# Kernel optimization log

Hardware: AMD Instinct MI355X
Metric: run time of the kernel (lower is better)

## Reference

```python
import jax, jax.numpy as jnp
import numpy as np

A = -0.75  # torch bicubic coefficient
K = 5
K2 = K * K
IN_CH = 32 * 2 + 169 + 16 * 2 + 1  # 266
TIMESTEP = 0.5


def _cubic_w(t):
    # t in [0,1); weights for taps at offsets -1,0,1,2 (torch cubic convolution, A=-0.75)
    w1 = ((A + 2.0) * t - (A + 3.0)) * t * t + 1.0
    s = 1.0 - t
    w2 = ((A + 2.0) * s - (A + 3.0)) * s * s + 1.0
    u = t + 1.0
    w0 = ((A * u - 5.0 * A) * u + 8.0 * A) * u - 4.0 * A
    v = 2.0 - t
    w3 = ((A * v - 5.0 * A) * v + 8.0 * A) * v - 4.0 * A
    return (w0, w1, w2, w3)


def _conv3(x, w, b):
    y = jax.lax.conv_general_dilated(x, w, (1, 1), 'SAME',
                                     dimension_numbers=('NCHW', 'OIHW', 'NCHW'))
    return y + b[None, :, None, None]


def _lrelu(x):
    return jnp.where(x >= 0, x, 0.1 * x)


def _kernel_pred(x, w1, b1, w2, b2, w3, b3, ow, ob, ww, wb):
    f = _lrelu(_conv3(x, w1, b1))
    f = _lrelu(_conv3(f, w2, b2))
    f = _lrelu(_conv3(f, w3, b3))
    offsets = _conv3(f, ow, ob)                      # (B, 2*K2, H, W)
    weights = jax.nn.softmax(_conv3(f, ww, wb), axis=1)  # (B, K2, H, W)
    return offsets, weights


def _adacof_sample(image, offsets, weights):
    # bicubic grid_sample(padding_mode='border', align_corners=True) + weighted combine
    b, c, h, w = image.shape
    k2 = weights.shape[1]
    gx = jnp.arange(w, dtype=image.dtype)
    gy = jnp.arange(h, dtype=image.dtype)
    dx = offsets[:, 0::2]                # (b,k2,h,w)
    dy = offsets[:, 1::2]
    # with align_corners=True, normalize->unnormalize is identity
    sx = gx[None, None, None, :] + dx
    sy = gy[None, None, :, None] + dy
    x0 = jnp.floor(sx); tx = sx - x0
    y0 = jnp.floor(sy); ty = sy - y0
    wx = _cubic_w(tx)
    wy = _cubic_w(ty)
    xi = [jnp.clip(x0 + (i - 1.0), 0, w - 1).astype(jnp.int32) for i in range(4)]
    yi = [jnp.clip(y0 + (i - 1.0), 0, h - 1).astype(jnp.int32) for i in range(4)]
    imgf = image.reshape(b, c, h * w)
    gather = jax.vmap(lambda im, idx: im[:, idx])   # (c,hw),(n,)->(c,n)
    acc = jnp.zeros((b, c, k2, h, w), image.dtype)
    for i in range(4):
        for j in range(4):
            idx = (yi[i] * w + xi[j]).reshape(b, -1)
            g = gather(imgf, idx).reshape(b, c, k2, h, w)
            acc = acc + g * (wy[i] * wx[j])[:, None]
    return jnp.einsum('bckhw,bkhw->bchw', acc, weights)


def setup_inputs() -> dict:
    key = jax.random.key(0)
    ks = iter(jax.random.split(key, 64))
    d = {}
    d['frame1'] = jax.random.normal(next(ks), (2, 3, 256, 256), jnp.float32)
    d['frame2'] = jax.random.normal(next(ks), (2, 3, 256, 256), jnp.float32)
    d['feat1'] = jax.random.normal(next(ks), (2, 32, 256, 256), jnp.float32)
    d['feat2'] = jax.random.normal(next(ks), (2, 32, 256, 256), jnp.float32)
    d['corr'] = jax.random.normal(next(ks), (2, 169, 256, 256), jnp.float32)

    def conv_w(o, i):
        return jax.random.normal(next(ks), (o, i, 3, 3), jnp.float32) * 0.05

    # full-res encoder
    d['fr_w1'] = conv_w(16, 3); d['fr_b1'] = jnp.zeros((16,), jnp.float32)
    d['fr_w2'] = conv_w(16, 16); d['fr_b2'] = jnp.zeros((16,), jnp.float32)
    # default grid offsets for offset_head bias (dx,dy interleaved)
    off_bias = []
    for i in range(K):
        for j in range(K):
            off_bias.extend([j - K // 2, i - K // 2])
    off_bias = jnp.asarray(off_bias, jnp.float32)
    for p in ('kp1', 'kp2'):
        d[p + '_w1'] = conv_w(256, IN_CH); d[p + '_b1'] = jnp.zeros((256,), jnp.float32)
        d[p + '_w2'] = conv_w(256, 256); d[p + '_b2'] = jnp.zeros((256,), jnp.float32)
        d[p + '_w3'] = conv_w(128, 256); d[p + '_b3'] = jnp.zeros((128,), jnp.float32)
        d[p + '_ow'] = jax.random.normal(next(ks), (2 * K2, 128, 3, 3), jnp.float32) * 0.01
        d[p + '_ob'] = off_bias
        d[p + '_ww'] = jax.random.normal(next(ks), (K2, 128, 3, 3), jnp.float32) * 0.01
        d[p + '_wb'] = jnp.full((K2,), 1.0 / K2, jnp.float32)
    d['bl_w1'] = conv_w(64, IN_CH); d['bl_b1'] = jnp.zeros((64,), jnp.float32)
    d['bl_w2'] = conv_w(1, 64); d['bl_b2'] = jnp.zeros((1,), jnp.float32)
    return d


def reference(frame1, frame2, feat1, feat2, corr,
              fr_w1, fr_b1, fr_w2, fr_b2,
              kp1_w1, kp1_b1, kp1_w2, kp1_b2, kp1_w3, kp1_b3, kp1_ow, kp1_ob, kp1_ww, kp1_wb,
              kp2_w1, kp2_b1, kp2_w2, kp2_b2, kp2_w3, kp2_b3, kp2_ow, kp2_ob, kp2_ww, kp2_wb,
              bl_w1, bl_b1, bl_w2, bl_b2):
    b, _, h, w = frame1.shape
    fr1 = _lrelu(_conv3(_lrelu(_conv3(frame1, fr_w1, fr_b1)), fr_w2, fr_b2))
    fr2 = _lrelu(_conv3(_lrelu(_conv3(frame2, fr_w1, fr_b1)), fr_w2, fr_b2))
    t_map = jnp.full((b, 1, h, w), TIMESTEP, frame1.dtype)
    combined = jnp.concatenate([feat1, feat2, corr, fr1, fr2, t_map], axis=1)
    offsets1, weights1 = _kernel_pred(combined, kp1_w1, kp1_b1, kp1_w2, kp1_b2,
                                      kp1_w3, kp1_b3, kp1_ow, kp1_ob, kp1_ww, kp1_wb)
    offsets2, weights2 = _kernel_pred(combined, kp2_w1, kp2_b1, kp2_w2, kp2_b2,
                                      kp2_w3, kp2_b3, kp2_ow, kp2_ob, kp2_ww, kp2_wb)
    sample1 = _adacof_sample(frame1, offsets1, weights1)
    sample2 = _adacof_sample(frame2, offsets2, weights2)
    blend = jax.nn.sigmoid(_conv3(_lrelu(_conv3(combined, bl_w1, bl_b1)), bl_w2, bl_b2))
    output = blend * sample1 + (1.0 - blend) * sample2
    return (output, blend, offsets1, offsets2, weights1, weights2)
```

## Files before the change

kernel.cpp:

```cpp
#include <hip/hip_runtime.h>
#include <cstdint>
#include <cstddef>

#define H 256
#define W 256
#define HW (H*W)
#define BATCH 2
#define CIN_TILE 4

typedef __bf16 bf16x8 __attribute__((ext_vector_type(8)));
typedef float f32x4 __attribute__((ext_vector_type(4)));
typedef __attribute__((address_space(1))) uint32_t gu32_t;
typedef __attribute__((address_space(3))) uint32_t lu32_t;

__device__ __forceinline__ void async16(const void* g, void* l) {
  __builtin_amdgcn_global_load_lds((const gu32_t*)g, (lu32_t*)l, 16, 0, 0);
}

__device__ __forceinline__ ushort f2bf(float f) {
  uint u = __float_as_uint(f);
  return (ushort)((u + 0x7FFFu + ((u >> 16) & 1u)) >> 16);
}
__device__ __forceinline__ float lrelu_f(float v) { return v >= 0.f ? v : 0.1f * v; }

#define SWN (2304 * 8)
#define SBN (4 * 640 * 8)
#define DYN_LDS_BYTES (2 * (SWN + SBN) * 2)

#define ISSUE_TAP(tt, bb)                                                     \
  do {                                                                        \
    asm volatile("ds_read_b128 %0, %1 offset:%c2"                             \
                 : "=v"(Afr[bb][0]) : "v"(aA0), "i"((tt) * 4096));            \
    asm volatile("ds_read_b128 %0, %1 offset:%c2"                             \
                 : "=v"(Afr[bb][1]) : "v"(aA1), "i"((tt) * 4096));            \
    asm volatile("ds_read_b128 %0, %1 offset:%c2"                             \
                 : "=v"(Afr[bb][2]) : "v"(aA2), "i"((tt) * 4096));            \
    asm volatile("ds_read_b128 %0, %1 offset:%c2"                             \
                 : "=v"(Afr[bb][3]) : "v"(aA3), "i"((tt) * 4096));            \
    asm volatile("ds_read_b128 %0, %1 offset:%c2"                             \
                 : "=v"(Bfr[bb][0]) : "v"(aB0),                               \
                   "i"(((((tt) / 3) * 34) + ((tt) % 3)) * 16));               \
    asm volatile("ds_read_b128 %0, %1 offset:%c2"                             \
                 : "=v"(Bfr[bb][1]) : "v"(aB1),                               \
                   "i"(((((tt) / 3) * 34) + ((tt) % 3)) * 16));               \
    asm volatile("ds_read_b128 %0, %1 offset:%c2"                             \
                 : "=v"(Bfr[bb][2]) : "v"(aB2),                               \
                   "i"(((((tt) / 3) * 34) + ((tt) % 3)) * 16));               \
    asm volatile("ds_read_b128 %0, %1 offset:%c2"                             \
                 : "=v"(Bfr[bb][3]) : "v"(aB3),                               \
                   "i"(((((tt) / 3) * 34) + ((tt) % 3)) * 16));               \
  } while (0)

template<int EPI>
__global__ __launch_bounds__(512) void convmm_k(
    const ushort* __restrict__ act, const ushort* __restrict__ wgt,
    const float* __restrict__ bias, ushort* __restrict__ dstb,
    float* __restrict__ dsto, float* __restrict__ dstw,
    const ushort* __restrict__ zpage, int Cin, int CoutS,
    int astride, int wstride, int bstride, int dstride)
{
  extern __shared__ __align__(16) ushort s_dyn[];

  const int z = blockIdx.z;
  act += (size_t)z * astride;
  wgt += (size_t)z * wstride;
  bias += (size_t)z * bstride;
  if constexpr (EPI == 0) dstb += (size_t)z * dstride;
  else { dsto += (size_t)z * (BATCH * 50 * HW); dstw += (size_t)z * (BATCH * 25 * HW); }

  const int tid = threadIdx.x;
  const int sp = blockIdx.x;
  const int bx = (sp & 7) * 32, by = (sp >> 3) * 16;
  const int co0 = blockIdx.y * 64;
  const int wv = tid >> 6, lane = tid & 63;
  const int c = lane & 15, kq = lane >> 4;
  const int oy = wv * 2;

  int wsrc[5];
#pragma unroll
  for (int it = 0; it < 5; ++it) {
    int i = tid + it * 512;
    if (i < 2304) {
      int co = i & 63, tk = i >> 6, tap = tk >> 2, kg = tk & 3;
      wsrc[it] = ((co0 + co) * 9 + tap) * Cin + kg * 8;
    } else wsrc[it] = 0;
  }
  int bsrc[5];
#pragma unroll
  for (int it = 0; it < 5; ++it) {
    int i = tid + it * 512;
    int kg = i / 640, px = i - kg * 640;
    int row = px / 34, xx = px - row * 34;
    int gy = by + row - 1, gx = bx + xx - 1;
    bool ok = (px < 612) && ((unsigned)gy < (unsigned)H) && ((unsigned)gx < (unsigned)W);
    bsrc[it] = ok ? ((gy * W + gx) * Cin + kg * 8) : -1;
  }

  auto stage = [&](int buf, int c0) {
    ushort* swc = s_dyn + (buf ? (SWN + SBN) : 0);
    ushort* sbc = swc + SWN;
#pragma unroll
    for (int it = 0; it < 5; ++it)
      if (it < 4 || tid < 2304 - 4 * 512)
        async16(wgt + wsrc[it] + c0, &swc[(size_t)(tid + it * 512) * 8]);
#pragma unroll
    for (int it = 0; it < 5; ++it) {
      const ushort* g = (bsrc[it] < 0) ? zpage : (act + bsrc[it] + c0);
      async16(g, &sbc[(size_t)(tid + it * 512) * 8]);
    }
  };

  f32x4 acc[4][4];
#pragma unroll
  for (int a = 0; a < 4; ++a)
#pragma unroll
    for (int b2 = 0; b2 < 4; ++b2) acc[a][b2] = (f32x4){0.f, 0.f, 0.f, 0.f};

  stage(0, 0);
  __syncthreads();

  const uint sdyn_base = (uint)(uintptr_t)(lu32_t*)s_dyn;

  const int nch = Cin >> 5;
  int cur = 0;
  for (int ch = 0; ch < nch; ++ch) {
    if (ch + 1 < nch) stage(cur ^ 1, (ch + 1) << 5);
    __builtin_amdgcn_sched_barrier(0);

    const uint swoff = sdyn_base + (cur ? (uint)((SWN + SBN) * 2) : 0u);
    const uint sboff = swoff + (uint)(SWN * 2);
    const uint aA0 = swoff + (uint)((kq * 64 + 0 * 16 + c) * 16);
    const uint aA1 = swoff + (uint)((kq * 64 + 1 * 16 + c) * 16);
    const uint aA2 = swoff + (uint)((kq * 64 + 2 * 16 + c) * 16);
    const uint aA3 = swoff + (uint)((kq * 64 + 3 * 16 + c) * 16);
    const uint aB0 = sboff + (uint)((kq * 640 + (oy + 0) * 34 + 0 * 16 + c) * 16);
    const uint aB1 = sboff + (uint)((kq * 640 + (oy + 0) * 34 + 1 * 16 + c) * 16);
    const uint aB2 = sboff + (uint)((kq * 640 + (oy + 1) * 34 + 0 * 16 + c) * 16);
    const uint aB3 = sboff + (uint)((kq * 640 + (oy + 1) * 34 + 1 * 16 + c) * 16);

    bf16x8 Afr[2][4], Bfr[2][4];
    ISSUE_TAP(0, 0);

#pragma unroll
    for (int t = 0; t < 9; ++t) {
      if (t < 8) {
        switch (t + 1) {
          case 1: ISSUE_TAP(1, 1); break;
          case 2: ISSUE_TAP(2, 0); break;
          case 3: ISSUE_TAP(3, 1); break;
          case 4: ISSUE_TAP(4, 0); break;
          case 5: ISSUE_TAP(5, 1); break;
          case 6: ISSUE_TAP(6, 0); break;
          case 7: ISSUE_TAP(7, 1); break;
          case 8: ISSUE_TAP(8, 0); break;
        }
        asm volatile("s_waitcnt lgkmcnt(8)" ::: "memory");
      } else {
        asm volatile("s_waitcnt lgkmcnt(0)" ::: "memory");
      }
      __builtin_amdgcn_sched_barrier(0);
      __builtin_amdgcn_s_setprio(1);
#pragma unroll
      for (int cf = 0; cf < 4; ++cf) {
#pragma unroll
        for (int pf = 0; pf < 4; ++pf)
          acc[cf][pf] = __builtin_amdgcn_mfma_f32_16x16x32_bf16(
              Afr[t & 1][cf], Bfr[t & 1][pf], acc[cf][pf], 0, 0, 0);
      }
      __builtin_amdgcn_s_setprio(0);
      __builtin_amdgcn_sched_barrier(0);
    }

    __syncthreads();
    cur ^= 1;
  }

  const int r4 = kq * 4;
#pragma unroll
  for (int cf = 0; cf < 4; ++cf) {
    int cob = co0 + cf * 16 + r4;
#pragma unroll
    for (int pf = 0; pf < 4; ++pf) {
      int gx2 = bx + (pf & 1) * 16 + c;
      int gy2 = by + oy + (pf >> 1);
      int gpix = gy2 * W + gx2;
      f32x4 v = acc[cf][pf];
      const float4 bv = *(const float4*)&bias[cob];
      if constexpr (EPI == 0) {
        ushort4 ov;
        float f0 = lrelu_f(v[0] + bv.x);
        float f1 = lrelu_f(v[1] + bv.y);
        float f2 = lrelu_f(v[2] + bv.z);
        float f3 = lrelu_f(v[3] + bv.w);
        ov.x = f2bf(f0); ov.y = f2bf(f1); ov.z = f2bf(f2); ov.w = f2bf(f3);
        *(ushort4*)&dstb[(size_t)gpix * CoutS + cob] = ov;
      } else {
        const float* bvp = &bv.x;
#pragma unroll
        for (int r = 0; r < 4; ++r) {
          int coa = cob + r;
          if (coa < 75) {
            float f = v[r] + bvp[r];
            if (coa < 50) dsto[(size_t)coa * HW + gpix] = f;
            else          dstw[(size_t)(coa - 50) * HW + gpix] = f;
          }
        }
      }
    }
  }
}

template<int CIN>
__global__ __launch_bounds__(256) void conv_fr_k(
    const float* __restrict__ sA, const float* __restrict__ sB, int mode,
    const float* __restrict__ wgt, const float* __restrict__ bias,
    float* __restrict__ dst)
{
  const int z = blockIdx.y;
  const float* src = (mode == 0)
      ? (((z >> 1) ? sB : sA) + (size_t)(z & 1) * 3 * HW)
      : (sA + (size_t)z * 16 * HW);
  float* out = dst + (size_t)z * 16 * HW;

  const int sp = blockIdx.x;
  const int bx = (sp & 7) * 32, by = (sp >> 3) * 32;
  const int tid = threadIdx.x;
  const int tx = tid & 15, ty = tid >> 4;

  __shared__ float s_in[CIN_TILE][34][36];
  float acc[16][2][2];
#pragma unroll
  for (int co = 0; co < 16; ++co) {
    acc[co][0][0] = 0.f; acc[co][0][1] = 0.f;
    acc[co][1][0] = 0.f; acc[co][1][1] = 0.f;
  }

  for (int c0 = 0; c0 < CIN; c0 += CIN_TILE) {
    __syncthreads();
    const int nst = CIN_TILE * 34 * 34;
    for (int i = tid; i < nst; i += 256) {
      int ci = i / (34 * 34);
      int r = i - ci * (34 * 34);
      int yy = r / 34;
      int xx = r - yy * 34;
      int gy = by + yy - 1, gx = bx + xx - 1;
      int cc = c0 + ci;
      float v = 0.f;
      if (cc < CIN && (unsigned)gy < (unsigned)H && (unsigned)gx < (unsigned)W)
        v = src[(size_t)cc * HW + gy * W + gx];
      s_in[ci][yy][xx] = v;
    }
    __syncthreads();

    const int cmax = (CIN - c0 < CIN_TILE) ? (CIN - c0) : CIN_TILE;
    for (int ci = 0; ci < cmax; ++ci) {
      float win[4][4];
#pragma unroll
      for (int iy = 0; iy < 4; ++iy)
#pragma unroll
        for (int ix = 0; ix < 4; ++ix)
          win[iy][ix] = s_in[ci][2 * ty + iy][2 * tx + ix];
#pragma unroll
      for (int co = 0; co < 16; ++co) {
        const float* wp = wgt + ((size_t)co * CIN + (c0 + ci)) * 9;
        float w0 = wp[0], w1 = wp[1], w2 = wp[2];
        float w3 = wp[3], w4 = wp[4], w5 = wp[5];
        float w6 = wp[6], w7 = wp[7], w8 = wp[8];
#pragma unroll
        for (int py = 0; py < 2; ++py)
#pragma unroll
          for (int px = 0; px < 2; ++px) {
            float s = acc[co][py][px];
            s += w0 * win[py + 0][px + 0];
            s += w1 * win[py + 0][px + 1];
            s += w2 * win[py + 0][px + 2];
            s += w3 * win[py + 1][px + 0];
            s += w4 * win[py + 1][px + 1];
            s += w5 * win[py + 1][px + 2];
            s += w6 * win[py + 2][px + 0];
            s += w7 * win[py + 2][px + 1];
            s += w8 * win[py + 2][px + 2];
            acc[co][py][px] = s;
          }
      }
    }
  }
#pragma unroll
  for (int co = 0; co < 16; ++co) {
    float bv = bias[co];
#pragma unroll
    for (int py = 0; py < 2; ++py)
#pragma unroll
      for (int px = 0; px < 2; ++px)
        out[(size_t)co * HW + (size_t)(by + 2 * ty + py) * W + (bx + 2 * tx + px)] =
            lrelu_f(acc[co][py][px] + bv);
  }
}

__global__ __launch_bounds__(256) void pack_k(
    const float* __restrict__ feat1, const float* __restrict__ feat2,
    const float* __restrict__ corr, const float* __restrict__ fr,
    ushort* __restrict__ comb, int b)
{
  int gid = blockIdx.x * 256 + threadIdx.x;
  int chunk = gid / HW;
  int p = gid - chunk * HW;
  int c0 = chunk * 32;

  uint u[16];
#pragma unroll
  for (int j = 0; j < 32; j += 2) {
    float f[2];
#pragma unroll
    for (int q = 0; q < 2; ++q) {
      int cc = c0 + j + q;
      float v;
      if (cc < 32)       v = feat1[(size_t)(b * 32 + cc) * HW + p];
      else if (cc < 64)  v = feat2[(size_t)(b * 32 + cc - 32) * HW + p];
      else if (cc < 233) v = corr[(size_t)(b * 169 + cc - 64) * HW + p];
      else if (cc < 249) v = fr[(size_t)(b * 16 + (cc - 233)) * HW + p];
      else if (cc < 265) v = fr[(size_t)((2 + b) * 16 + (cc - 249)) * HW + p];
      else if (cc == 265) v = 0.5f;
      else               v = 0.f;
      f[q] = v;
    }
    u[j >> 1] = (uint)f2bf(f[0]) | ((uint)f2bf(f[1]) << 16);
  }
  uint4* dst = (uint4*)&comb[(size_t)p * 288 + c0];
#pragma unroll
  for (int q = 0; q < 4; ++q) {
    uint4 t;
    t.x = u[q * 4 + 0]; t.y = u[q * 4 + 1]; t.z = u[q * 4 + 2]; t.w = u[q * 4 + 3];
    dst[q] = t;
  }
}

struct PrepSeg { const float* src; ushort* dst; int O, I, Ipad; };
struct PrepArgs { PrepSeg s[13]; int pre[14]; };

__global__ __launch_bounds__(256) void prep_all_k(PrepArgs a)
{
  int gid = blockIdx.x * 256 + threadIdx.x;
  if (gid >= a.pre[13]) return;
  int si = 0;
  while (gid >= a.pre[si + 1]) ++si;
  int idx = gid - a.pre[si];
  const PrepSeg sg = a.s[si];
  int i = idx % sg.Ipad;
  int r = idx / sg.Ipad;
  int tap = r % 9;
  int o = r / 9;
  float v = (i < sg.I) ? sg.src[((size_t)o * sg.I + i) * 9 + tap] : 0.f;
  sg.dst[idx] = f2bf(v);
}

__global__ __launch_bounds__(256) void bias_all_k(
    const float* kb1_0, const float* kb1_1, const float* kb2_0, const float* kb2_1,
    const float* kb3_0, const float* kb3_1,
    const float* ob0, const float* wb0, const float* ob1, const float* wb1,
    float* bb1, float* bb2, float* bb3, float* bbh)
{
  int yq = blockIdx.y;
  int i = threadIdx.x;
  switch (yq) {
    case 0: bb1[i] = kb1_0[i]; break;
    case 1: bb1[256 + i] = kb1_1[i]; break;
    case 2: bb2[i] = kb2_0[i]; break;
    case 3: bb2[256 + i] = kb2_1[i]; break;
    case 4: if (i < 128) bb3[i] = kb3_0[i]; break;
    case 5: if (i < 128) bb3[128 + i] = kb3_1[i]; break;
    case 6: if (i < 128) bbh[i]       = (i < 50) ? ob0[i] : ((i < 75) ? wb0[i - 50] : 0.f); break;
    case 7: if (i < 128) bbh[128 + i] = (i < 50) ? ob1[i] : ((i < 75) ? wb1[i - 50] : 0.f); break;
  }
}

__global__ __launch_bounds__(256) void blend2_k(
    const ushort* __restrict__ actD, const float* __restrict__ wgt,
    const float* __restrict__ b2, float* __restrict__ outp)
{
  int p = blockIdx.x * 256 + threadIdx.x;
  int y = p >> 8, x = p & 255;
  float acc = b2[0];
  for (int dy = -1; dy <= 1; ++dy) {
    int gy = y + dy;
    if ((unsigned)gy >= (unsigned)H) continue;
    for (int dx = -1; dx <= 1; ++dx) {
      int gx = x + dx;
      if ((unsigned)gx >= (unsigned)W) continue;
      int tap = (dy + 1) * 3 + (dx + 1);
      const ushort* rowp = actD + (size_t)(gy * W + gx) * 64;
#pragma unroll
      for (int c8 = 0; c8 < 8; ++c8) {
        uint4 v = *(const uint4*)&rowp[c8 * 8];
        const uint* vv = &v.x;
#pragma unroll
        for (int q = 0; q < 4; ++q) {
          float f0 = __uint_as_float(vv[q] << 16);
          float f1 = __uint_as_float(vv[q] & 0xFFFF0000u);
          int ci = c8 * 8 + q * 2;
          acc += f0 * wgt[ci * 9 + tap];
          acc += f1 * wgt[(ci + 1) * 9 + tap];
        }
      }
    }
  }
  outp[p] = 1.f / (1.f + expf(-acc));
}

__global__ __launch_bounds__(256) void softmax25_k(float* __restrict__ w1,
                                                   float* __restrict__ w2)
{
  float* wr = blockIdx.y ? w2 : w1;
  int p = blockIdx.x * 256 + threadIdx.x;
  if (p >= HW) return;
  float v[25];
  float m = -1e30f;
#pragma unroll
  for (int k = 0; k < 25; ++k) {
    v[k] = wr[(size_t)k * HW + p];
    m = fmaxf(m, v[k]);
  }
  float s = 0.f;
#pragma unroll
  for (int k = 0; k < 25; ++k) {
    v[k] = expf(v[k] - m);
    s += v[k];
  }
  float inv = 1.f / s;
#pragma unroll
  for (int k = 0; k < 25; ++k)
    wr[(size_t)k * HW + p] = v[k] * inv;
}

__device__ __forceinline__ void cubic4(float t, float* cw)
{
  const float A_ = -0.75f;
  float t2 = t * t;
  cw[1] = ((A_ + 2.f) * t - (A_ + 3.f)) * t2 + 1.f;
  float s = 1.f - t;
  cw[2] = ((A_ + 2.f) * s - (A_ + 3.f)) * (s * s) + 1.f;
  float u = t + 1.f;
  cw[0] = ((A_ * u - 5.f * A_) * u + 8.f * A_) * u - 4.f * A_;
  float v = 2.f - t;
  cw[3] = ((A_ * v - 5.f * A_) * v + 8.f * A_) * v - 4.f * A_;
}

#define ATW 64
#define ATH 4
#define AHL 8
#define AROWS (ATH + 2*AHL)
#define ACOLS (ATW + 2*AHL)

__global__ __launch_bounds__(256) void adacof_final_k(
    const float* __restrict__ frame1, const float* __restrict__ frame2,
    const float* __restrict__ off1, const float* __restrict__ off2,
    const float* __restrict__ wt1, const float* __restrict__ wt2,
    const float* __restrict__ blend, float* __restrict__ outp)
{
  __shared__ __align__(16) float4 s_img[2 * AROWS * ACOLS];

  const int tid = threadIdx.x;
  int t = blockIdx.x;
  const int tilesPerImg = (H / ATH) * (W / ATW);
  const int b = t / tilesPerImg; t -= b * tilesPerImg;
  const int by = (t >> 2) * ATH, bx = (t & 3) * ATW;
  const int ty = tid >> 6, txx = tid & 63;
  const int y = by + ty, x = bx + txx;
  const int p = y * W + x;
  const int tx0 = bx - AHL, ty0 = by - AHL;

  const float* f1 = frame1 + (size_t)b * 3 * HW;
  const float* f2 = frame2 + (size_t)b * 3 * HW;

  for (int i = tid; i < AROWS * ACOLS; i += 256) {
    int r = i / ACOLS, cc = i - r * ACOLS;
    int gy = min(max(ty0 + r, 0), H - 1);
    int gx = min(max(tx0 + cc, 0), W - 1);
    int q = gy * W + gx;
    float4 v1, v2;
    v1.x = f1[q]; v1.y = f1[HW + q]; v1.z = f1[2 * HW + q]; v1.w = 0.f;
    v2.x = f2[q]; v2.y = f2[HW + q]; v2.z = f2[2 * HW + q]; v2.w = 0.f;
    s_img[i] = v1;
    s_img[AROWS * ACOLS + i] = v2;
  }
  __syncthreads();

  float a1[3] = {0.f, 0.f, 0.f};
  float a2[3] = {0.f, 0.f, 0.f};

  const size_t ob1 = (size_t)b * 50 * HW, wb1 = (size_t)b * 25 * HW;

#pragma unroll 2
  for (int k = 0; k < 25; ++k) {
#pragma unroll
    for (int fr = 0; fr < 2; ++fr) {
      const float* off = fr ? off2 : off1;
      const float* wts = fr ? wt2 : wt1;
      const float* img = fr ? f2 : f1;
      float* acc = fr ? a2 : a1;

      float dx = off[ob1 + (size_t)(2 * k) * HW + p];
      float dy = off[ob1 + (size_t)(2 * k + 1) * HW + p];
      float wk = wts[wb1 + (size_t)k * HW + p];
      float sx = (float)x + dx, sy = (float)y + dy;
      float x0f = floorf(sx), y0f = floorf(sy);
      float tx = sx - x0f, tyf = sy - y0f;
      float wx[4], wy[4];
      cubic4(tx, wx);
      cubic4(tyf, wy);
      int ix0 = (int)x0f, iy0 = (int)y0f;

      bool inT = (ix0 - 1 >= tx0) && (ix0 + 2 <= tx0 + ACOLS - 1) &&
                 (iy0 - 1 >= ty0) && (iy0 + 2 <= ty0 + AROWS - 1);
      if (__builtin_expect(inT, 1)) {
        const float4* base = &s_img[(size_t)fr * AROWS * ACOLS +
                                    (iy0 - 1 - ty0) * ACOLS + (ix0 - 1 - tx0)];
#pragma unroll
        for (int i = 0; i < 4; ++i) {
#pragma unroll
          for (int j = 0; j < 4; ++j) {
            float wf = wy[i] * wx[j] * wk;
            float4 v = base[i * ACOLS + j];
            acc[0] += v.x * wf;
            acc[1] += v.y * wf;
            acc[2] += v.z * wf;
          }
        }
      } else {
        int xi[4], yi[4];
#pragma unroll
        for (int i = 0; i < 4; ++i) {
          xi[i] = min(max(ix0 + i - 1, 0), W - 1);
          yi[i] = min(max(iy0 + i - 1, 0), H - 1);
        }
#pragma unroll
        for (int i = 0; i < 4; ++i) {
#pragma unroll
          for (int j = 0; j < 4; ++j) {
            float wf = wy[i] * wx[j] * wk;
            int q = yi[i] * W + xi[j];
            acc[0] += img[q] * wf;
            acc[1] += img[HW + q] * wf;
            acc[2] += img[2 * HW + q] * wf;
          }
        }
      }
    }
  }

  float bl = blend[(size_t)b * HW + p];
#pragma unroll
  for (int c3 = 0; c3 < 3; ++c3)
    outp[((size_t)b * 3 + c3) * HW + p] = bl * a1[c3] + (1.f - bl) * a2[c3];
}

extern "C" void kernel_launch(void* const* d_in, const int* in_sizes, int n_in,
                              void* d_out, int out_size, void* d_ws, size_t ws_size,
                              hipStream_t stream)
{
  const float* frame1 = (const float*)d_in[0];
  const float* frame2 = (const float*)d_in[1];
  const float* feat1  = (const float*)d_in[2];
  const float* feat2  = (const float*)d_in[3];
  const float* corr   = (const float*)d_in[4];
  const float* fr_w1  = (const float*)d_in[5];
  const float* fr_b1  = (const float*)d_in[6];
  const float* fr_w2  = (const float*)d_in[7];
  const float* fr_b2  = (const float*)d_in[8];

  const float* kw1[2] = {(const float*)d_in[9],  (const float*)d_in[19]};
  const float* kb1[2] = {(const float*)d_in[10], (const float*)d_in[20]};
  const float* kw2[2] = {(const float*)d_in[11], (const float*)d_in[21]};
  const float* kb2[2] = {(const float*)d_in[12], (const float*)d_in[22]};
  const float* kw3[2] = {(const float*)d_in[13], (const float*)d_in[23]};
  const float* kb3[2] = {(const float*)d_in[14], (const float*)d_in[24]};
  const float* kow[2] = {(const float*)d_in[15], (const float*)d_in[25]};
  const float* kob[2] = {(const float*)d_in[16], (const float*)d_in[26]};
  const float* kww[2] = {(const float*)d_in[17], (const float*)d_in[27]};
  const float* kwb[2] = {(const float*)d_in[18], (const float*)d_in[28]};

  const float* bl_w1 = (const float*)d_in[29];
  const float* bl_b1 = (const float*)d_in[30];
  const float* bl_w2 = (const float*)d_in[31];
  const float* bl_b2 = (const float*)d_in[32];

  float* out = (float*)d_out;
  float* o_out   = out;
  float* o_blend = o_out   + (size_t)BATCH * 3 * HW;
  float* o_off1  = o_blend + (size_t)BATCH * 1 * HW;
  float* o_off2  = o_off1  + (size_t)BATCH * 50 * HW;
  float* o_w1    = o_off2  + (size_t)BATCH * 50 * HW;
  float* o_w2    = o_w1    + (size_t)BATCH * 25 * HW;

  hipFuncSetAttribute((const void*)convmm_k<0>,
                      hipFuncAttributeMaxDynamicSharedMemorySize, DYN_LDS_BYTES);
  hipFuncSetAttribute((const void*)convmm_k<1>,
                      hipFuncAttributeMaxDynamicSharedMemorySize, DYN_LDS_BYTES);

  size_t off = 0;
  char* wsb = (char*)d_ws;
  auto alloc = [&](size_t bytes) -> void* {
    void* pp = wsb + off;
    off += (bytes + 255) & ~(size_t)255;
    return pp;
  };
  const size_t NEED_MERGED = 212700000;
  const bool merged = ws_size >= NEED_MERGED;
  const int NZ = merged ? 2 : 1;

  ushort* zpage = (ushort*)alloc(512);
  ushort* wp1   = (ushort*)alloc((size_t)2 * 256 * 9 * 288 * 2);
  ushort* wp2   = (ushort*)alloc((size_t)2 * 256 * 9 * 256 * 2);
  ushort* wp3   = (ushort*)alloc((size_t)2 * 128 * 9 * 256 * 2);
  ushort* wph   = (ushort*)alloc((size_t)2 * 128 * 9 * 128 * 2);
  ushort* wpb   = (ushort*)alloc((size_t)64 * 9 * 288 * 2);
  float*  bb1   = (float*)alloc(2 * 256 * 4);
  float*  bb2   = (float*)alloc(2 * 256 * 4);
  float*  bb3   = (float*)alloc(2 * 128 * 4);
  float*  bbh   = (float*)alloc(2 * 128 * 4);
  float*  tmp4  = (float*)alloc((size_t)4 * 16 * HW * 4);
  float*  frbuf = (float*)alloc((size_t)4 * 16 * HW * 4);
  ushort* comb  = (ushort*)alloc((size_t)HW * 288 * 2);
  ushort* actA  = (ushort*)alloc((size_t)NZ * HW * 256 * 2);
  ushort* actB  = (ushort*)alloc((size_t)NZ * HW * 256 * 2);

  dim3 blk(256);
  dim3 cblk(512);

  hipMemsetAsync(zpage, 0, 512, stream);
  {
    PrepArgs pa;
    const int W1 = 256 * 9 * 288, W2 = 256 * 9 * 256, W3 = 128 * 9 * 256;
    const int OW = 50 * 9 * 128, WW = 25 * 9 * 128, ZW = 53 * 9 * 128;
    const int WB = 64 * 9 * 288;
    const int HP = 128 * 9 * 128;
    PrepSeg segs[13] = {
      {kw1[0], wp1,                    256, 266, 288},
      {kw1[1], wp1 + W1,               256, 266, 288},
      {kw2[0], wp2,                    256, 256, 256},
      {kw2[1], wp2 + W2,               256, 256, 256},
      {kw3[0], wp3,                    128, 256, 256},
      {kw3[1], wp3 + W3,               128, 256, 256},
      {kow[0], wph,                     50, 128, 128},
      {kww[0], wph + OW,                25, 128, 128},
      {nullptr, wph + OW + WW,          53,   0, 128},
      {kow[1], wph + HP,                50, 128, 128},
      {kww[1], wph + HP + OW,           25, 128, 128},
      {nullptr, wph + HP + OW + WW,     53,   0, 128},
      {bl_w1,  wpb,                     64, 266, 288},
    };
    int tots[13] = {W1, W1, W2, W2, W3, W3, OW, WW, ZW, OW, WW, ZW, WB};
    pa.pre[0] = 0;
    for (int s = 0; s < 13; ++s) { pa.s[s] = segs[s]; pa.pre[s + 1] = pa.pre[s] + tots[s]; }
    int nblk = (pa.pre[13] + 255) / 256;
    prep_all_k<<<dim3(nblk), blk, 0, stream>>>(pa);
  }
  bias_all_k<<<dim3(1, 8), blk, 0, stream>>>(kb1[0], kb1[1], kb2[0], kb2[1],
                                             kb3[0], kb3[1], kob[0], kwb[0],
                                             kob[1], kwb[1], bb1, bb2, bb3, bbh);

  conv_fr_k<3><<<dim3(64, 4), blk, 0, stream>>>(frame1, frame2, 0, fr_w1, fr_b1, tmp4);
  conv_fr_k<16><<<dim3(64, 4), blk, 0, stream>>>(tmp4, nullptr, 1, fr_w2, fr_b2, frbuf);

  const int W1 = 256 * 9 * 288, W2 = 256 * 9 * 256, W3 = 128 * 9 * 256;
  const int HP = 128 * 9 * 128;

  for (int b = 0; b < BATCH; ++b) {
    pack_k<<<dim3(9 * HW / 256), blk, 0, stream>>>(feat1, feat2, corr, frbuf, comb, b);

    for (int pp = 0; pp < 2 / NZ; ++pp) {
      const size_t po = pp;
      convmm_k<0><<<dim3(128, 4, NZ), cblk, DYN_LDS_BYTES, stream>>>(
          comb, wp1 + po * W1, bb1 + po * 256, actA + po * (size_t)HW * 256,
          nullptr, nullptr, zpage, 288, 256, 0, W1, 256, HW * 256);
      convmm_k<0><<<dim3(128, 4, NZ), cblk, DYN_LDS_BYTES, stream>>>(
          actA + po * (size_t)HW * 256, wp2 + po * W2, bb2 + po * 256,
          actB + po * (size_t)HW * 256,
          nullptr, nullptr, zpage, 256, 256, HW * 256, W2, 256, HW * 256);
      convmm_k<0><<<dim3(128, 2, NZ), cblk, DYN_LDS_BYTES, stream>>>(
          actB + po * (size_t)HW * 256, wp3 + po * W3, bb3 + po * 128,
          actA + po * (size_t)HW * 128,
          nullptr, nullptr, zpage, 256, 128, HW * 256, W3, 128, HW * 128);
      convmm_k<1><<<dim3(128, 2, NZ), cblk, DYN_LDS_BYTES, stream>>>(
          actA + po * (size_t)HW * 128, wph + po * HP, bbh + po * 128, nullptr,
          o_off1 + (size_t)b * 50 * HW + po * (size_t)BATCH * 50 * HW,
          o_w1 + (size_t)b * 25 * HW + po * (size_t)BATCH * 25 * HW,
          zpage, 128, 0, HW * 128, HP, 128, 0);
    }
    softmax25_k<<<dim3(HW / 256, 2), blk, 0, stream>>>(
        o_w1 + (size_t)b * 25 * HW, o_w2 + (size_t)b * 25 * HW);

    convmm_k<0><<<dim3(128, 1, 1), cblk, DYN_LDS_BYTES, stream>>>(
        comb, wpb, bl_b1, actB, nullptr, nullptr, zpage, 288, 64, 0, 0, 0, 0);
    blend2_k<<<dim3(HW / 256), blk, 0, stream>>>(actB, bl_w2, bl_b2,
                                                 o_blend + (size_t)b * HW);
  }

  adacof_final_k<<<dim3(BATCH * (H / ATH) * (W / ATW)), blk, 0, stream>>>(
      frame1, frame2, o_off1, o_off2, o_w1, o_w2, o_blend, o_out);
}
```

Before: 1.302 ms.

## Batch both images and both predictors into single conv launches when workspace allows

Adds a workspace tier that, when the workspace is large enough, packs both batch images at once. Each conv layer then runs as a single launch with grid z covering predictor×batch (4 slices), and softmax and blend are batched the same way. The goal is fewer kernel launches and more blocks per launch for better CU occupancy on the conv GEMMs. It needs a larger workspace for activations, and falls back to the old per-batch path otherwise.

```diff
diff --git a/kernel.cpp b/kernel.cpp
--- a/kernel.cpp
+++ b/kernel.cpp
@@ -57,16 +57,21 @@
     const float* __restrict__ bias, ushort* __restrict__ dstb,
     float* __restrict__ dsto, float* __restrict__ dstw,
     const ushort* __restrict__ zpage, int Cin, int CoutS,
-    int astride, int wstride, int bstride, int dstride)
+    int pdim, int aP, int aB, int wP, int bP, int dP, int dB)
 {
   extern __shared__ __align__(16) ushort s_dyn[];
 
-  const int z = blockIdx.z;
-  act += (size_t)z * astride;
-  wgt += (size_t)z * wstride;
-  bias += (size_t)z * bstride;
-  if constexpr (EPI == 0) dstb += (size_t)z * dstride;
-  else { dsto += (size_t)z * (BATCH * 50 * HW); dstw += (size_t)z * (BATCH * 25 * HW); }
+  const int zp = (int)(blockIdx.z % (unsigned)pdim);
+  const int zb = (int)(blockIdx.z / (unsigned)pdim);
+  act += (size_t)zp * aP + (size_t)zb * aB;
+  wgt += (size_t)zp * wP;
+  bias += (size_t)zp * bP;
+  if constexpr (EPI == 0) {
+    dstb += (size_t)zp * dP + (size_t)zb * dB;
+  } else {
+    dsto += (size_t)zp * (BATCH * 50 * HW) + (size_t)zb * (50 * HW);
+    dstw += (size_t)zp * (BATCH * 25 * HW) + (size_t)zb * (25 * HW);
+  }
 
   const int tid = threadIdx.x;
   const int sp = blockIdx.x;
@@ -300,12 +305,15 @@
 __global__ __launch_bounds__(256) void pack_k(
     const float* __restrict__ feat1, const float* __restrict__ feat2,
     const float* __restrict__ corr, const float* __restrict__ fr,
-    ushort* __restrict__ comb, int b)
+    ushort* __restrict__ comb, int b0)
 {
   int gid = blockIdx.x * 256 + threadIdx.x;
-  int chunk = gid / HW;
-  int p = gid - chunk * HW;
+  int bb = gid / (9 * HW);
+  int rem = gid - bb * (9 * HW);
+  int chunk = rem / HW;
+  int p = rem - chunk * HW;
   int c0 = chunk * 32;
+  int b = b0 + bb;
 
   uint u[16];
 #pragma unroll
@@ -326,7 +334,7 @@
     }
     u[j >> 1] = (uint)f2bf(f[0]) | ((uint)f2bf(f[1]) << 16);
   }
-  uint4* dst = (uint4*)&comb[(size_t)p * 288 + c0];
+  uint4* dst = (uint4*)&comb[(size_t)bb * HW * 288 + (size_t)p * 288 + c0];
 #pragma unroll
   for (int q = 0; q < 4; ++q) {
     uint4 t;
@@ -378,6 +386,8 @@
     const ushort* __restrict__ actD, const float* __restrict__ wgt,
     const float* __restrict__ b2, float* __restrict__ outp)
 {
+  actD += (size_t)blockIdx.y * HW * 64;
+  outp += (size_t)blockIdx.y * HW;
   int p = blockIdx.x * 256 + threadIdx.x;
   int y = p >> 8, x = p & 255;
   float acc = b2[0];
@@ -410,7 +420,8 @@
 __global__ __launch_bounds__(256) void softmax25_k(float* __restrict__ w1,
                                                    float* __restrict__ w2)
 {
-  float* wr = blockIdx.y ? w2 : w1;
+  int yq = blockIdx.y;
+  float* wr = ((yq & 1) ? w2 : w1) + (size_t)(yq >> 1) * 25 * HW;
   int p = blockIdx.x * 256 + threadIdx.x;
   if (p >= HW) return;
   float v[25];
@@ -597,6 +608,12 @@
   hipFuncSetAttribute((const void*)convmm_k<1>,
                       hipFuncAttributeMaxDynamicSharedMemorySize, DYN_LDS_BYTES);
 
+  const size_t NEED_FULL   = 386000000;
+  const size_t NEED_MERGED = 212700000;
+  const int tier = (ws_size >= NEED_FULL) ? 2 : (ws_size >= NEED_MERGED ? 1 : 0);
+  const int NACT = (tier == 2) ? 4 : (tier == 1 ? 2 : 1);
+  const int NCMB = (tier == 2) ? 2 : 1;
+
   size_t off = 0;
   char* wsb = (char*)d_ws;
   auto alloc = [&](size_t bytes) -> void* {
@@ -604,9 +621,6 @@
     off += (bytes + 255) & ~(size_t)255;
     return pp;
   };
-  const size_t NEED_MERGED = 212700000;
-  const bool merged = ws_size >= NEED_MERGED;
-  const int NZ = merged ? 2 : 1;
 
   ushort* zpage = (ushort*)alloc(512);
   ushort* wp1   = (ushort*)alloc((size_t)2 * 256 * 9 * 288 * 2);
@@ -620,20 +634,22 @@
   float*  bbh   = (float*)alloc(2 * 128 * 4);
   float*  tmp4  = (float*)alloc((size_t)4 * 16 * HW * 4);
   float*  frbuf = (float*)alloc((size_t)4 * 16 * HW * 4);
-  ushort* comb  = (ushort*)alloc((size_t)HW * 288 * 2);
-  ushort* actA  = (ushort*)alloc((size_t)NZ * HW * 256 * 2);
-  ushort* actB  = (ushort*)alloc((size_t)NZ * HW * 256 * 2);
+  ushort* comb  = (ushort*)alloc((size_t)NCMB * HW * 288 * 2);
+  ushort* actA  = (ushort*)alloc((size_t)NACT * HW * 256 * 2);
+  ushort* actB  = (ushort*)alloc((size_t)NACT * HW * 256 * 2);
 
   dim3 blk(256);
   dim3 cblk(512);
+
+  const int W1 = 256 * 9 * 288, W2 = 256 * 9 * 256, W3 = 128 * 9 * 256;
+  const int HP = 128 * 9 * 128;
+  const int CS = HW * 288;
 
   hipMemsetAsync(zpage, 0, 512, stream);
   {
     PrepArgs pa;
-    const int W1 = 256 * 9 * 288, W2 = 256 * 9 * 256, W3 = 128 * 9 * 256;
     const int OW = 50 * 9 * 128, WW = 25 * 9 * 128, ZW = 53 * 9 * 128;
     const int WB = 64 * 9 * 288;
-    const int HP = 128 * 9 * 128;
     PrepSeg segs[13] = {
       {kw1[0], wp1,                    256, 266, 288},
       {kw1[1], wp1 + W1,               256, 266, 288},
@@ -662,38 +678,62 @@
   conv_fr_k<3><<<dim3(64, 4), blk, 0, stream>>>(frame1, frame2, 0, fr_w1, fr_b1, tmp4);
   conv_fr_k<16><<<dim3(64, 4), blk, 0, stream>>>(tmp4, nullptr, 1, fr_w2, fr_b2, frbuf);
 
-  const int W1 = 256 * 9 * 288, W2 = 256 * 9 * 256, W3 = 128 * 9 * 256;
-  const int HP = 128 * 9 * 128;
-
-  for (int b = 0; b < BATCH; ++b) {
-    pack_k<<<dim3(9 * HW / 256), blk, 0, stream>>>(feat1, feat2, corr, frbuf, comb, b);
-
-    for (int pp = 0; pp < 2 / NZ; ++pp) {
-      const size_t po = pp;
-      convmm_k<0><<<dim3(128, 4, NZ), cblk, DYN_LDS_BYTES, stream>>>(
-          comb, wp1 + po * W1, bb1 + po * 256, actA + po * (size_t)HW * 256,
-          nullptr, nullptr, zpage, 288, 256, 0, W1, 256, HW * 256);
-      convmm_k<0><<<dim3(128, 4, NZ), cblk, DYN_LDS_BYTES, stream>>>(
-          actA + po * (size_t)HW * 256, wp2 + po * W2, bb2 + po * 256,
-          actB + po * (size_t)HW * 256,
-          nullptr, nullptr, zpage, 256, 256, HW * 256, W2, 256, HW * 256);
-      convmm_k<0><<<dim3(128, 2, NZ), cblk, DYN_LDS_BYTES, stream>>>(
-          actB + po * (size_t)HW * 256, wp3 + po * W3, bb3 + po * 128,
-          actA + po * (size_t)HW * 128,
-          nullptr, nullptr, zpage, 256, 128, HW * 256, W3, 128, HW * 128);
-      convmm_k<1><<<dim3(128, 2, NZ), cblk, DYN_LDS_BYTES, stream>>>(
-          actA + po * (size_t)HW * 128, wph + po * HP, bbh + po * 128, nullptr,
-          o_off1 + (size_t)b * 50 * HW + po * (size_t)BATCH * 50 * HW,
-          o_w1 + (size_t)b * 25 * HW + po * (size_t)BATCH * 25 * HW,
-          zpage, 128, 0, HW * 128, HP, 128, 0);
-    }
-    softmax25_k<<<dim3(HW / 256, 2), blk, 0, stream>>>(
-        o_w1 + (size_t)b * 25 * HW, o_w2 + (size_t)b * 25 * HW);
-
-    convmm_k<0><<<dim3(128, 1, 1), cblk, DYN_LDS_BYTES, stream>>>(
-        comb, wpb, bl_b1, actB, nullptr, nullptr, zpage, 288, 64, 0, 0, 0, 0);
-    blend2_k<<<dim3(HW / 256), blk, 0, stream>>>(actB, bl_w2, bl_b2,
-                                                 o_blend + (size_t)b * HW);
+  if (tier == 2) {
+    pack_k<<<dim3(2 * 9 * HW / 256), blk, 0, stream>>>(feat1, feat2, corr, frbuf, comb, 0);
+
+    convmm_k<0><<<dim3(128, 4, 4), cblk, DYN_LDS_BYTES, stream>>>(
+        comb, wp1, bb1, actA, nullptr, nullptr, zpage, 288, 256,
+        2, 0, CS, W1, 256, HW * 256, 2 * HW * 256);
+    convmm_k<0><<<dim3(128, 4, 4), cblk, DYN_LDS_BYTES, stream>>>(
+        actA, wp2, bb2, actB, nullptr, nullptr, zpage, 256, 256,
+        2, HW * 256, 2 * HW * 256, W2, 256, HW * 256, 2 * HW * 256);
+    convmm_k<0><<<dim3(128, 2, 4), cblk, DYN_LDS_BYTES, stream>>>(
+        actB, wp3, bb3, actA, nullptr, nullptr, zpage, 256, 128,
+        2, HW * 256, 2 * HW * 256, W3, 128, HW * 128, 2 * HW * 128);
+    convmm_k<1><<<dim3(128, 2, 4), cblk, DYN_LDS_BYTES, stream>>>(
+        actA, wph, bbh, nullptr, o_off1, o_w1, zpage, 128, 0,
+        2, HW * 128, 2 * HW * 128, HP, 128, 0, 0);
+    softmax25_k<<<dim3(HW / 256, 4), blk, 0, stream>>>(o_w1, o_w2);
+
+    convmm_k<0><<<dim3(128, 1, 2), cblk, DYN_LDS_BYTES, stream>>>(
+        comb, wpb, bl_b1, actB, nullptr, nullptr, zpage, 288, 64,
+        1, 0, CS, 0, 0, 0, HW * 64);
+    blend2_k<<<dim3(HW / 256, 2), blk, 0, stream>>>(actB, bl_w2, bl_b2, o_blend);
+  } else {
+    const int NZ = (tier == 1) ? 2 : 1;
+    for (int b = 0; b < BATCH; ++b) {
+      pack_k<<<dim3(9 * HW / 256), blk, 0, stream>>>(feat1, feat2, corr, frbuf, comb, b);
+
+      for (int pp = 0; pp < 2 / NZ; ++pp) {
+        const size_t po = pp;
+        convmm_k<0><<<dim3(128, 4, NZ), cblk, DYN_LDS_BYTES, stream>>>(
+            comb, wp1 + po * W1, bb1 + po * 256, actA + po * (size_t)HW * 256,
+            nullptr, nullptr, zpage, 288, 256,
+            2, 0, 0, W1, 256, HW * 256, 0);
+        convmm_k<0><<<dim3(128, 4, NZ), cblk, DYN_LDS_BYTES, stream>>>(
+            actA + po * (size_t)HW * 256, wp2 + po * W2, bb2 + po * 256,
+            actB + po * (size_t)HW * 256, nullptr, nullptr, zpage, 256, 256,
+            2, HW * 256, 0, W2, 256, HW * 256, 0);
+        convmm_k<0><<<dim3(128, 2, NZ), cblk, DYN_LDS_BYTES, stream>>>(
+            actB + po * (size_t)HW * 256, wp3 + po * W3, bb3 + po * 128,
+            actA + po * (size_t)HW * 128, nullptr, nullptr, zpage, 256, 128,
+            2, HW * 256, 0, W3, 128, HW * 128, 0);
+        convmm_k<1><<<dim3(128, 2, NZ), cblk, DYN_LDS_BYTES, stream>>>(
+            actA + po * (size_t)HW * 128, wph + po * HP, bbh + po * 128, nullptr,
+            o_off1 + (size_t)b * 50 * HW + po * (size_t)BATCH * 50 * HW,
+            o_w1 + (size_t)b * 25 * HW + po * (size_t)BATCH * 25 * HW,
+            zpage, 128, 0,
+            2, HW * 128, 0, HP, 128, 0, 0);
+      }
+      softmax25_k<<<dim3(HW / 256, 2), blk, 0, stream>>>(
+          o_w1 + (size_t)b * 25 * HW, o_w2 + (size_t)b * 25 * HW);
+
+      convmm_k<0><<<dim3(128, 1, 1), cblk, DYN_LDS_BYTES, stream>>>(
+          comb, wpb, bl_b1, actB, nullptr, nullptr, zpage, 288, 64,
+          1, 0, 0, 0, 0, 0, 0);
+      blend2_k<<<dim3(HW / 256, 1), blk, 0, stream>>>(actB, bl_w2, bl_b2,
+                                                      o_blend + (size_t)b * HW);
+    }
   }
 
   adacof_final_k<<<dim3(BATCH * (H / ATH) * (W / ATW)), blk, 0, stream>>>(
```

Result: no change. 1.302 ms (+0.0%).
